# Performance work log

Measured on AMD Instinct MI355X. Metric: run time of the kernel, lower is better.

Reference implementation:

```python
import jax, jax.numpy as jnp
import numpy as np

N, IN_F, OUT_F = 8192, 512, 128
NEG = -1e11
LRELU_SLOPE = 0.01  # torch nn.LeakyReLU default


def setup_inputs() -> dict:
    key = jax.random.key(0)
    k1, k2, k3, k4, k5 = jax.random.split(key, 5)
    h = jax.random.normal(k1, (N, IN_F), dtype=jnp.float32)
    adj = jax.random.randint(k2, (N, N), 0, 2, dtype=jnp.int32)
    # nn.Linear weights, [out, in] convention; kaiming-uniform-ish init
    w = jax.random.uniform(k3, (OUT_F, IN_F), dtype=jnp.float32,
                           minval=-1.0, maxval=1.0) / np.sqrt(IN_F)
    a1 = jax.random.uniform(k4, (1, OUT_F), dtype=jnp.float32,
                            minval=-1.0, maxval=1.0) / np.sqrt(OUT_F)
    a2 = jax.random.uniform(k5, (1, OUT_F), dtype=jnp.float32,
                            minval=-1.0, maxval=1.0) / np.sqrt(OUT_F)
    return {"h": h, "adj": adj, "w": w, "a1": a1, "a2": a2}


def reference(h, adj, w, a1, a2):
    wh = h @ w.T                                # [N, out]
    wh1 = wh @ a1.T                             # [N, 1]
    wh2 = wh @ a2.T                             # [N, 1]
    e = wh1 + wh2.T                             # [N, N] broadcast add
    e = jnp.where(e > 0, e, LRELU_SLOPE * e)    # leaky relu
    scores = jnp.where(adj > 0, e, jnp.float32(NEG))
    attention = jax.nn.softmax(scores, axis=-1)  # [N, N]
    h_new = attention @ wh                       # [N, out]
    return jax.nn.elu(h_new)
```

## Files before the change

### kernel.cpp

```cpp
#include <hip/hip_runtime.h>
#include <hip/hip_bf16.h>
#include <cstdint>
#include <cstddef>

#define NV    8192
#define KIN   512
#define MOUT  128
#define LOG2E 1.4426950408889634f

typedef __attribute__((ext_vector_type(4))) float f32x4;
typedef __attribute__((ext_vector_type(8))) short short8;

__device__ __forceinline__ float elu1(float x) { return x > 0.f ? x : expm1f(x); }

__device__ __forceinline__ unsigned int pkbf2(float a, float b) {
  union { __hip_bfloat162 h2; unsigned int u; } r;
  r.h2 = __float22bfloat162_rn(make_float2(a, b));
  return r.u;
}

__global__ __launch_bounds__(256) void k_wh(const float* __restrict__ h,
                                            const float* __restrict__ w,
                                            const float* __restrict__ a1,
                                            const float* __restrict__ a2,
                                            unsigned short* __restrict__ fragB,
                                            float* __restrict__ wh1,
                                            float* __restrict__ wh2) {
  __shared__ __align__(16) float hT[64][36];
  __shared__ __align__(16) float wT[64][128];
  const int t = threadIdx.x;
  const int row0 = blockIdx.x * 32;
  const int hr = t >> 3, hu = t & 7;
  const int wc = t >> 1, whalf = t & 1;
  const int cg = t & 31, rg = t >> 5;
  const int c0 = cg * 4, r0 = rg * 4;
  float acc[4][4] = {};

  for (int kt = 0; kt < 8; ++kt) {
    const int k0 = kt * 64;
    __syncthreads();
#pragma unroll
    for (int v = 0; v < 8; ++v)
      hT[hu + 8 * v][hr] = h[(size_t)(row0 + hr) * KIN + k0 + hu + 8 * v];
#pragma unroll
    for (int mv = 0; mv < 8; ++mv) {
      const float4 wv4 = *(const float4*)&w[(size_t)wc * KIN + k0 + whalf * 32 + mv * 4];
      wT[whalf * 32 + mv * 4 + 0][wc] = wv4.x;
      wT[whalf * 32 + mv * 4 + 1][wc] = wv4.y;
      wT[whalf * 32 + mv * 4 + 2][wc] = wv4.z;
      wT[whalf * 32 + mv * 4 + 3][wc] = wv4.w;
    }
    __syncthreads();
#pragma unroll 8
    for (int kk = 0; kk < 64; ++kk) {
      const float4 hv = *(const float4*)&hT[kk][r0];
      const float4 wv4 = *(const float4*)&wT[kk][c0];
      const float hvv[4] = {hv.x, hv.y, hv.z, hv.w};
      const float wvv[4] = {wv4.x, wv4.y, wv4.z, wv4.w};
#pragma unroll
      for (int i = 0; i < 4; ++i)
#pragma unroll
        for (int j = 0; j < 4; ++j)
          acc[i][j] = fmaf(hvv[i], wvv[j], acc[i][j]);
    }
  }

  {
    const size_t jt = (size_t)(row0 >> 6);
    const int ks = (row0 >> 5) & 1;
    const int lg = rg >> 1, ebase = (rg & 1) * 4;
    const int cgf = cg >> 2;
    const size_t fbase = (((jt * 8 + cgf) * 2 + ks) * 64 + lg * 16) * 8 + ebase;
#pragma unroll
    for (int j = 0; j < 4; ++j) {
      const int l15 = (cg & 3) * 4 + j;
      uint2 o;
      o.x = pkbf2(acc[0][j], acc[1][j]);
      o.y = pkbf2(acc[2][j], acc[3][j]);
      *(uint2*)&fragB[fbase + (size_t)l15 * 8] = o;
    }
  }

  const float4 a1v = *(const float4*)&a1[c0];
  const float4 a2v = *(const float4*)&a2[c0];
#pragma unroll
  for (int i = 0; i < 4; ++i) {
    float s1 = acc[i][0] * a1v.x + acc[i][1] * a1v.y + acc[i][2] * a1v.z + acc[i][3] * a1v.w;
    float s2 = acc[i][0] * a2v.x + acc[i][1] * a2v.y + acc[i][2] * a2v.z + acc[i][3] * a2v.w;
#pragma unroll
    for (int off = 16; off > 0; off >>= 1) {
      s1 += __shfl_down(s1, off, 32);
      s2 += __shfl_down(s2, off, 32);
    }
    if (cg == 0) {
      wh1[row0 + r0 + i] = s1 * LOG2E;
      wh2[row0 + r0 + i] = s2 * LOG2E;
    }
  }
}

__global__ __launch_bounds__(256, 4) void k_attn_p(const unsigned short* __restrict__ fragB,
                                                   const int* __restrict__ adj,
                                                   const float* __restrict__ wh1l,
                                                   const float* __restrict__ wh2l,
                                                   float* __restrict__ out_p,
                                                   float* __restrict__ psum_p,
                                                   int ntiles) {
  extern __shared__ char smem[];
  const int t = threadIdx.x;
  const int i0 = blockIdx.x * 64;
  const int jbase = blockIdx.y * ntiles * 64;
  const int lane = t & 63, wv = t >> 6;
  const int ih = wv & 1, ch = wv >> 1;
  const int l15 = lane & 15, lg = lane >> 4;
  const int mstride = ntiles * 8 + 8;

  {
    const int nchunk = ntiles >> 4;
    for (int rr = 0; rr < 16; ++rr) {
      const int r = wv * 16 + rr;
      const int* ap = adj + (size_t)(i0 + r) * NV + jbase;
      for (int c = 0; c < nchunk; ++c) {
        const int chunk = c * 64 + lane;
        const int* bp = ap + chunk * 16;
        const int4 v0 = *(const int4*)(bp);
        const int4 v1 = *(const int4*)(bp + 4);
        const int4 v2 = *(const int4*)(bp + 8);
        const int4 v3 = *(const int4*)(bp + 12);
        const unsigned int m =
            (unsigned)(v0.x & 1)        | ((unsigned)(v0.y & 1) << 1)  |
            ((unsigned)(v0.z & 1) << 2) | ((unsigned)(v0.w & 1) << 3)  |
            ((unsigned)(v1.x & 1) << 4) | ((unsigned)(v1.y & 1) << 5)  |
            ((unsigned)(v1.z & 1) << 6) | ((unsigned)(v1.w & 1) << 7)  |
            ((unsigned)(v2.x & 1) << 8) | ((unsigned)(v2.y & 1) << 9)  |
            ((unsigned)(v2.z & 1) << 10)| ((unsigned)(v2.w & 1) << 11) |
            ((unsigned)(v3.x & 1) << 12)| ((unsigned)(v3.y & 1) << 13) |
            ((unsigned)(v3.z & 1) << 14)| ((unsigned)(v3.w & 1) << 15);
        *(unsigned short*)&smem[r * mstride + chunk * 2] = (unsigned short)m;
      }
    }
  }
  __syncthreads();

  const int rb = ih * 32;
  const float wh1a = wh1l[i0 + rb + l15];
  const float wh1b = wh1l[i0 + rb + 16 + l15];
  const char* mrowa = smem + (rb + l15) * mstride;
  const char* mrowb = smem + (rb + 16 + l15) * mstride;
  const unsigned short* bptr = fragB + (size_t)(jbase >> 6) * 8192 + ch * 4096 + lane * 8;
  const float* w2ptr = wh2l + jbase + lg * 8;

  f32x4 acc[2][4] = {};
  f32x4 accs[2] = {};
  short8 onesf;
#pragma unroll
  for (int e = 0; e < 8; ++e) onesf[e] = (short)0x3F80;

  uint2 m2a = *(const uint2*)&mrowa[0];
  uint2 m2b = *(const uint2*)&mrowb[0];
  short8 bf[8];
#pragma unroll
  for (int ks = 0; ks < 2; ++ks)
#pragma unroll
    for (int cgl = 0; cgl < 4; ++cgl)
      bf[ks * 4 + cgl] = *(const short8*)(bptr + cgl * 1024 + ks * 512);
  bptr += 8192;

  for (int it = 0; it < ntiles; ++it) {
    const unsigned int m16a = ((m2a.x >> (8 * lg)) & 0xFFu) |
                              (((m2a.y >> (8 * lg)) & 0xFFu) << 8);
    const unsigned int m16b = ((m2b.x >> (8 * lg)) & 0xFFu) |
                              (((m2b.y >> (8 * lg)) & 0xFFu) << 8);
    const float4 wq0 = *(const float4*)(w2ptr);
    const float4 wq1 = *(const float4*)(w2ptr + 4);
    const float4 wq2 = *(const float4*)(w2ptr + 32);
    const float4 wq3 = *(const float4*)(w2ptr + 36);
    w2ptr += 64;

    short8 afa[2], afb[2];
#pragma unroll
    for (int ks = 0; ks < 2; ++ks) {
      const float4 wa = ks ? wq2 : wq0;
      const float4 wb = ks ? wq3 : wq1;
      const float w2v[8] = {wa.x, wa.y, wa.z, wa.w, wb.x, wb.y, wb.z, wb.w};
      union { short8 s8; unsigned int u[4]; } pka, pkb;
#pragma unroll
      for (int e = 0; e < 4; ++e) {
        const float x0 = wh1a + w2v[2 * e];
        const float x1 = wh1a + w2v[2 * e + 1];
        const float y0 = wh1b + w2v[2 * e];
        const float y1 = wh1b + w2v[2 * e + 1];
        const float lx0 = fmaxf(x0, 0.01f * x0);
        const float lx1 = fmaxf(x1, 0.01f * x1);
        const float ly0 = fmaxf(y0, 0.01f * y0);
        const float ly1 = fmaxf(y1, 0.01f * y1);
        float px0 = __builtin_amdgcn_exp2f(lx0);
        float px1 = __builtin_amdgcn_exp2f(lx1);
        float py0 = __builtin_amdgcn_exp2f(ly0);
        float py1 = __builtin_amdgcn_exp2f(ly1);
        px0 = ((m16a >> (ks * 8 + 2 * e)) & 1u) ? px0 : 0.f;
        px1 = ((m16a >> (ks * 8 + 2 * e + 1)) & 1u) ? px1 : 0.f;
        py0 = ((m16b >> (ks * 8 + 2 * e)) & 1u) ? py0 : 0.f;
        py1 = ((m16b >> (ks * 8 + 2 * e + 1)) & 1u) ? py1 : 0.f;
        pka.u[e] = pkbf2(px0, px1);
        pkb.u[e] = pkbf2(py0, py1);
      }
      afa[ks] = pka.s8;
      afb[ks] = pkb.s8;
    }
    if (it + 1 < ntiles) {
      m2a = *(const uint2*)&mrowa[(it + 1) * 8];
      m2b = *(const uint2*)&mrowb[(it + 1) * 8];
    }
#pragma unroll
    for (int ks = 0; ks < 2; ++ks) {
      acc[0][0] = __builtin_amdgcn_mfma_f32_16x16x32_bf16(afa[ks], bf[ks * 4 + 0], acc[0][0], 0, 0, 0);
      acc[0][1] = __builtin_amdgcn_mfma_f32_16x16x32_bf16(afa[ks], bf[ks * 4 + 1], acc[0][1], 0, 0, 0);
      acc[0][2] = __builtin_amdgcn_mfma_f32_16x16x32_bf16(afa[ks], bf[ks * 4 + 2], acc[0][2], 0, 0, 0);
      acc[0][3] = __builtin_amdgcn_mfma_f32_16x16x32_bf16(afa[ks], bf[ks * 4 + 3], acc[0][3], 0, 0, 0);
      accs[0]   = __builtin_amdgcn_mfma_f32_16x16x32_bf16(afa[ks], onesf, accs[0], 0, 0, 0);
      acc[1][0] = __builtin_amdgcn_mfma_f32_16x16x32_bf16(afb[ks], bf[ks * 4 + 0], acc[1][0], 0, 0, 0);
      acc[1][1] = __builtin_amdgcn_mfma_f32_16x16x32_bf16(afb[ks], bf[ks * 4 + 1], acc[1][1], 0, 0, 0);
      acc[1][2] = __builtin_amdgcn_mfma_f32_16x16x32_bf16(afb[ks], bf[ks * 4 + 2], acc[1][2], 0, 0, 0);
      acc[1][3] = __builtin_amdgcn_mfma_f32_16x16x32_bf16(afb[ks], bf[ks * 4 + 3], acc[1][3], 0, 0, 0);
      accs[1]   = __builtin_amdgcn_mfma_f32_16x16x32_bf16(afb[ks], onesf, accs[1], 0, 0, 0);
    }
    if (it + 1 < ntiles) {
#pragma unroll
      for (int ks = 0; ks < 2; ++ks)
#pragma unroll
        for (int cgl = 0; cgl < 4; ++cgl)
          bf[ks * 4 + cgl] = *(const short8*)(bptr + cgl * 1024 + ks * 512);
      bptr += 8192;
    }
  }

  if (ch == 0 && l15 == 0) {
#pragma unroll
    for (int rg = 0; rg < 2; ++rg)
#pragma unroll
      for (int r = 0; r < 4; ++r)
        psum_p[(size_t)blockIdx.y * NV + i0 + rb + rg * 16 + lg * 4 + r] = accs[rg][r];
  }

#pragma unroll
  for (int rg = 0; rg < 2; ++rg) {
    const size_t ob = ((size_t)blockIdx.y * NV + i0 + rb + rg * 16) * MOUT + ch * 64;
#pragma unroll
    for (int cgl = 0; cgl < 4; ++cgl)
#pragma unroll
      for (int r = 0; r < 4; ++r)
        out_p[ob + (size_t)(lg * 4 + r) * MOUT + cgl * 16 + l15] = acc[rg][cgl][r];
  }
}

__global__ __launch_bounds__(256) void k_comb(const float* __restrict__ out_p,
                                              const float* __restrict__ psum_p,
                                              float* __restrict__ out, int S) {
  const int idx = (blockIdx.x * 256 + threadIdx.x) * 4;
  const int n = idx >> 7;
  float denom = 0.f;
  for (int s = 0; s < S; ++s) denom += psum_p[(size_t)s * NV + n];
  float4 acc = {0.f, 0.f, 0.f, 0.f};
  for (int s = 0; s < S; ++s) {
    const float4 v = *(const float4*)&out_p[(size_t)s * NV * MOUT + idx];
    acc.x += v.x; acc.y += v.y; acc.z += v.z; acc.w += v.w;
  }
  const float inv = 1.f / denom;
  float4 o;
  o.x = elu1(acc.x * inv);
  o.y = elu1(acc.y * inv);
  o.z = elu1(acc.z * inv);
  o.w = elu1(acc.w * inv);
  *(float4*)&out[idx] = o;
}

extern "C" void kernel_launch(void* const* d_in, const int* in_sizes, int n_in,
                              void* d_out, int out_size, void* d_ws, size_t ws_size,
                              hipStream_t stream) {
  const float* h  = (const float*)d_in[0];
  const int* adj  = (const int*)d_in[1];
  const float* w  = (const float*)d_in[2];
  const float* a1 = (const float*)d_in[3];
  const float* a2 = (const float*)d_in[4];
  float* out = (float*)d_out;

  char* ws = (char*)d_ws;
  unsigned short* fragB = (unsigned short*)ws;
  size_t off = (size_t)MOUT * NV * 2;
  float* wh1 = (float*)(ws + off); off += (size_t)NV * 4;
  float* wh2 = (float*)(ws + off); off += (size_t)NV * 4;
  float* psum_p = (float*)(ws + off); off += (size_t)8 * NV * 4;
  float* out_p = (float*)(ws + off);

  int S = 8;
  while (S > 1 && off + (size_t)S * NV * MOUT * 4 > ws_size) S >>= 1;
  const int ntiles = 128 / S;
  const size_t smbytes = (size_t)64 * (ntiles * 8 + 8);

  k_wh<<<NV / 32, 256, 0, stream>>>(h, w, a1, a2, fragB, wh1, wh2);
  k_attn_p<<<dim3(NV / 64, S), 256, smbytes, stream>>>(fragB, adj, wh1, wh2, out_p, psum_p, ntiles);
  k_comb<<<(NV * MOUT / 4) / 256, 256, 0, stream>>>(out_p, psum_p, out, S);
}
```

Baseline: 130.4 us.

## Pipeline adjacency mask loads with MFMA compute in attention kernel

Replaces the up-front adjacency-to-bitmask prologue, which loaded all mask bits before any compute began, with a software pipeline. Groups of adjacency rows are issued into registers two groups ahead and written to shared memory in stages, with a barrier every four tiles, so adjacency streaming overlaps the exp/MFMA work. It also hardcodes the split factor to 8 and uses a fixed static shared buffer, dropping the workspace-size fallback and the occupancy hint of 4 in launch bounds. The B-fragment prefetch across iterations is removed, so B loads now happen inside each tile.

```diff
diff --git a/kernel.cpp b/kernel.cpp
--- a/kernel.cpp
+++ b/kernel.cpp
@@ -99,56 +99,69 @@
   }
 }
 
-__global__ __launch_bounds__(256, 4) void k_attn_p(const unsigned short* __restrict__ fragB,
-                                                   const int* __restrict__ adj,
-                                                   const float* __restrict__ wh1l,
-                                                   const float* __restrict__ wh2l,
-                                                   float* __restrict__ out_p,
-                                                   float* __restrict__ psum_p,
-                                                   int ntiles) {
-  extern __shared__ char smem[];
+__device__ __forceinline__ void issue_grp(const int* __restrict__ base, int G, int wv,
+                                          int lane, int4 (&dst)[4]) {
+  const int c = G >> 2, rb4 = (G & 3) * 4;
+  const int r = wv * 16 + rb4 + (lane >> 4);
+  const int* p = base + (size_t)r * NV + c * 256 + (lane & 15) * 16;
+  dst[0] = *(const int4*)(p);
+  dst[1] = *(const int4*)(p + 4);
+  dst[2] = *(const int4*)(p + 8);
+  dst[3] = *(const int4*)(p + 12);
+}
+
+__device__ __forceinline__ void write_grp(char* sm, int G, int wv, int lane,
+                                          const int4 (&src)[4]) {
+  const int c = G >> 2, rb4 = (G & 3) * 4;
+  const int r = wv * 16 + rb4 + (lane >> 4);
+  unsigned int us = 0;
+#pragma unroll
+  for (int m = 0; m < 4; ++m) {
+    us |= (unsigned)(src[m].x & 1) << (4 * m);
+    us |= (unsigned)(src[m].y & 1) << (4 * m + 1);
+    us |= (unsigned)(src[m].z & 1) << (4 * m + 2);
+    us |= (unsigned)(src[m].w & 1) << (4 * m + 3);
+  }
+  const int l15q = lane & 15;
+  const int tile = c * 4 + (l15q >> 2), slot = l15q & 3;
+  *(unsigned short*)&sm[r * 136 + tile * 8 + slot * 2] = (unsigned short)us;
+}
+
+__global__ __launch_bounds__(256) void k_attn_p(const unsigned short* __restrict__ fragB,
+                                                const int* __restrict__ adj,
+                                                const float* __restrict__ wh1l,
+                                                const float* __restrict__ wh2l,
+                                                float* __restrict__ out_p,
+                                                float* __restrict__ psum_p) {
+  __shared__ char smask[64 * 136];
   const int t = threadIdx.x;
   const int i0 = blockIdx.x * 64;
-  const int jbase = blockIdx.y * ntiles * 64;
+  const int jbase = blockIdx.y * 1024;
   const int lane = t & 63, wv = t >> 6;
   const int ih = wv & 1, ch = wv >> 1;
   const int l15 = lane & 15, lg = lane >> 4;
-  const int mstride = ntiles * 8 + 8;
-
-  {
-    const int nchunk = ntiles >> 4;
-    for (int rr = 0; rr < 16; ++rr) {
-      const int r = wv * 16 + rr;
-      const int* ap = adj + (size_t)(i0 + r) * NV + jbase;
-      for (int c = 0; c < nchunk; ++c) {
-        const int chunk = c * 64 + lane;
-        const int* bp = ap + chunk * 16;
-        const int4 v0 = *(const int4*)(bp);
-        const int4 v1 = *(const int4*)(bp + 4);
-        const int4 v2 = *(const int4*)(bp + 8);
-        const int4 v3 = *(const int4*)(bp + 12);
-        const unsigned int m =
-            (unsigned)(v0.x & 1)        | ((unsigned)(v0.y & 1) << 1)  |
-            ((unsigned)(v0.z & 1) << 2) | ((unsigned)(v0.w & 1) << 3)  |
-            ((unsigned)(v1.x & 1) << 4) | ((unsigned)(v1.y & 1) << 5)  |
-            ((unsigned)(v1.z & 1) << 6) | ((unsigned)(v1.w & 1) << 7)  |
-            ((unsigned)(v2.x & 1) << 8) | ((unsigned)(v2.y & 1) << 9)  |
-            ((unsigned)(v2.z & 1) << 10)| ((unsigned)(v2.w & 1) << 11) |
-            ((unsigned)(v3.x & 1) << 12)| ((unsigned)(v3.y & 1) << 13) |
-            ((unsigned)(v3.z & 1) << 14)| ((unsigned)(v3.w & 1) << 15);
-        *(unsigned short*)&smem[r * mstride + chunk * 2] = (unsigned short)m;
-      }
-    }
-  }
-  __syncthreads();
+
+  const int* abase = adj + (size_t)i0 * NV + jbase;
+
+  int4 ga[4], gb[4];
+  issue_grp(abase, 0, wv, lane, ga);
+  issue_grp(abase, 1, wv, lane, gb);
+  write_grp(smask, 0, wv, lane, ga);
+  issue_grp(abase, 2, wv, lane, ga);
+  write_grp(smask, 1, wv, lane, gb);
+  issue_grp(abase, 3, wv, lane, gb);
+  write_grp(smask, 2, wv, lane, ga);
+  issue_grp(abase, 4, wv, lane, ga);
+  write_grp(smask, 3, wv, lane, gb);
+  issue_grp(abase, 5, wv, lane, gb);
 
   const int rb = ih * 32;
   const float wh1a = wh1l[i0 + rb + l15];
   const float wh1b = wh1l[i0 + rb + 16 + l15];
-  const char* mrowa = smem + (rb + l15) * mstride;
-  const char* mrowb = smem + (rb + 16 + l15) * mstride;
-  const unsigned short* bptr = fragB + (size_t)(jbase >> 6) * 8192 + ch * 4096 + lane * 8;
-  const float* w2ptr = wh2l + jbase + lg * 8;
+  const char* mrowa = smask + (rb + l15) * 136;
+  const char* mrowb = smask + (rb + 16 + l15) * 136;
+  const unsigned short* bbase = fragB + (size_t)(jbase >> 6) * 8192 + ch * 4096 + lane * 8;
+  const float* w2base = wh2l + jbase + lg * 8;
 
   f32x4 acc[2][4] = {};
   f32x4 accs[2] = {};
@@ -156,82 +169,85 @@
 #pragma unroll
   for (int e = 0; e < 8; ++e) onesf[e] = (short)0x3F80;
 
-  uint2 m2a = *(const uint2*)&mrowa[0];
-  uint2 m2b = *(const uint2*)&mrowb[0];
-  short8 bf[8];
-#pragma unroll
-  for (int ks = 0; ks < 2; ++ks)
-#pragma unroll
-    for (int cgl = 0; cgl < 4; ++cgl)
-      bf[ks * 4 + cgl] = *(const short8*)(bptr + cgl * 1024 + ks * 512);
-  bptr += 8192;
-
-  for (int it = 0; it < ntiles; ++it) {
-    const unsigned int m16a = ((m2a.x >> (8 * lg)) & 0xFFu) |
-                              (((m2a.y >> (8 * lg)) & 0xFFu) << 8);
-    const unsigned int m16b = ((m2b.x >> (8 * lg)) & 0xFFu) |
-                              (((m2b.y >> (8 * lg)) & 0xFFu) << 8);
-    const float4 wq0 = *(const float4*)(w2ptr);
-    const float4 wq1 = *(const float4*)(w2ptr + 4);
-    const float4 wq2 = *(const float4*)(w2ptr + 32);
-    const float4 wq3 = *(const float4*)(w2ptr + 36);
-    w2ptr += 64;
-
-    short8 afa[2], afb[2];
-#pragma unroll
-    for (int ks = 0; ks < 2; ++ks) {
-      const float4 wa = ks ? wq2 : wq0;
-      const float4 wb = ks ? wq3 : wq1;
-      const float w2v[8] = {wa.x, wa.y, wa.z, wa.w, wb.x, wb.y, wb.z, wb.w};
-      union { short8 s8; unsigned int u[4]; } pka, pkb;
-#pragma unroll
-      for (int e = 0; e < 4; ++e) {
-        const float x0 = wh1a + w2v[2 * e];
-        const float x1 = wh1a + w2v[2 * e + 1];
-        const float y0 = wh1b + w2v[2 * e];
-        const float y1 = wh1b + w2v[2 * e + 1];
-        const float lx0 = fmaxf(x0, 0.01f * x0);
-        const float lx1 = fmaxf(x1, 0.01f * x1);
-        const float ly0 = fmaxf(y0, 0.01f * y0);
-        const float ly1 = fmaxf(y1, 0.01f * y1);
-        float px0 = __builtin_amdgcn_exp2f(lx0);
-        float px1 = __builtin_amdgcn_exp2f(lx1);
-        float py0 = __builtin_amdgcn_exp2f(ly0);
-        float py1 = __builtin_amdgcn_exp2f(ly1);
-        px0 = ((m16a >> (ks * 8 + 2 * e)) & 1u) ? px0 : 0.f;
-        px1 = ((m16a >> (ks * 8 + 2 * e + 1)) & 1u) ? px1 : 0.f;
-        py0 = ((m16b >> (ks * 8 + 2 * e)) & 1u) ? py0 : 0.f;
-        py1 = ((m16b >> (ks * 8 + 2 * e + 1)) & 1u) ? py1 : 0.f;
-        pka.u[e] = pkbf2(px0, px1);
-        pkb.u[e] = pkbf2(py0, py1);
+  for (int q = 0; q < 4; ++q) {
+    __syncthreads();
+#pragma unroll
+    for (int tt = 0; tt < 4; ++tt) {
+      const int T = q * 4 + tt;
+      if (T + 4 < 16) {
+        if ((tt & 1) == 0) {
+          write_grp(smask, T + 4, wv, lane, ga);
+          if (T + 6 < 16) issue_grp(abase, T + 6, wv, lane, ga);
+        } else {
+          write_grp(smask, T + 4, wv, lane, gb);
+          if (T + 6 < 16) issue_grp(abase, T + 6, wv, lane, gb);
+        }
       }
-      afa[ks] = pka.s8;
-      afb[ks] = pkb.s8;
-    }
-    if (it + 1 < ntiles) {
-      m2a = *(const uint2*)&mrowa[(it + 1) * 8];
-      m2b = *(const uint2*)&mrowb[(it + 1) * 8];
-    }
-#pragma unroll
-    for (int ks = 0; ks < 2; ++ks) {
-      acc[0][0] = __builtin_amdgcn_mfma_f32_16x16x32_bf16(afa[ks], bf[ks * 4 + 0], acc[0][0], 0, 0, 0);
-      acc[0][1] = __builtin_amdgcn_mfma_f32_16x16x32_bf16(afa[ks], bf[ks * 4 + 1], acc[0][1], 0, 0, 0);
-      acc[0][2] = __builtin_amdgcn_mfma_f32_16x16x32_bf16(afa[ks], bf[ks * 4 + 2], acc[0][2], 0, 0, 0);
-      acc[0][3] = __builtin_amdgcn_mfma_f32_16x16x32_bf16(afa[ks], bf[ks * 4 + 3], acc[0][3], 0, 0, 0);
-      accs[0]   = __builtin_amdgcn_mfma_f32_16x16x32_bf16(afa[ks], onesf, accs[0], 0, 0, 0);
-      acc[1][0] = __builtin_amdgcn_mfma_f32_16x16x32_bf16(afb[ks], bf[ks * 4 + 0], acc[1][0], 0, 0, 0);
-      acc[1][1] = __builtin_amdgcn_mfma_f32_16x16x32_bf16(afb[ks], bf[ks * 4 + 1], acc[1][1], 0, 0, 0);
-      acc[1][2] = __builtin_amdgcn_mfma_f32_16x16x32_bf16(afb[ks], bf[ks * 4 + 2], acc[1][2], 0, 0, 0);
-      acc[1][3] = __builtin_amdgcn_mfma_f32_16x16x32_bf16(afb[ks], bf[ks * 4 + 3], acc[1][3], 0, 0, 0);
-      accs[1]   = __builtin_amdgcn_mfma_f32_16x16x32_bf16(afb[ks], onesf, accs[1], 0, 0, 0);
-    }
-    if (it + 1 < ntiles) {
-#pragma unroll
-      for (int ks = 0; ks < 2; ++ks)
-#pragma unroll
-        for (int cgl = 0; cgl < 4; ++cgl)
-          bf[ks * 4 + cgl] = *(const short8*)(bptr + cgl * 1024 + ks * 512);
-      bptr += 8192;
+      short8 bf[8];
+      {
+        const unsigned short* bp = bbase + (size_t)T * 8192;
+#pragma unroll
+        for (int ks = 0; ks < 2; ++ks)
+#pragma unroll
+          for (int cgl = 0; cgl < 4; ++cgl)
+            bf[ks * 4 + cgl] = *(const short8*)(bp + cgl * 1024 + ks * 512);
+      }
+      const uint2 m2a = *(const uint2*)&mrowa[T * 8];
+      const uint2 m2b = *(const uint2*)&mrowb[T * 8];
+      const float* w2p = w2base + T * 64;
+      const float4 wq0 = *(const float4*)(w2p);
+      const float4 wq1 = *(const float4*)(w2p + 4);
+      const float4 wq2 = *(const float4*)(w2p + 32);
+      const float4 wq3 = *(const float4*)(w2p + 36);
+      const unsigned int m16a = ((m2a.x >> (8 * lg)) & 0xFFu) |
+                                (((m2a.y >> (8 * lg)) & 0xFFu) << 8);
+      const unsigned int m16b = ((m2b.x >> (8 * lg)) & 0xFFu) |
+                                (((m2b.y >> (8 * lg)) & 0xFFu) << 8);
+
+      short8 afa[2], afb[2];
+#pragma unroll
+      for (int ks = 0; ks < 2; ++ks) {
+        const float4 wa = ks ? wq2 : wq0;
+        const float4 wb = ks ? wq3 : wq1;
+        const float w2v[8] = {wa.x, wa.y, wa.z, wa.w, wb.x, wb.y, wb.z, wb.w};
+        union { short8 s8; unsigned int u[4]; } pka, pkb;
+#pragma unroll
+        for (int e = 0; e < 4; ++e) {
+          const float x0 = wh1a + w2v[2 * e];
+          const float x1 = wh1a + w2v[2 * e + 1];
+          const float y0 = wh1b + w2v[2 * e];
+          const float y1 = wh1b + w2v[2 * e + 1];
+          const float lx0 = fmaxf(x0, 0.01f * x0);
+          const float lx1 = fmaxf(x1, 0.01f * x1);
+          const float ly0 = fmaxf(y0, 0.01f * y0);
+          const float ly1 = fmaxf(y1, 0.01f * y1);
+          float px0 = __builtin_amdgcn_exp2f(lx0);
+          float px1 = __builtin_amdgcn_exp2f(lx1);
+          float py0 = __builtin_amdgcn_exp2f(ly0);
+          float py1 = __builtin_amdgcn_exp2f(ly1);
+          px0 = ((m16a >> (ks * 8 + 2 * e)) & 1u) ? px0 : 0.f;
+          px1 = ((m16a >> (ks * 8 + 2 * e + 1)) & 1u) ? px1 : 0.f;
+          py0 = ((m16b >> (ks * 8 + 2 * e)) & 1u) ? py0 : 0.f;
+          py1 = ((m16b >> (ks * 8 + 2 * e + 1)) & 1u) ? py1 : 0.f;
+          pka.u[e] = pkbf2(px0, px1);
+          pkb.u[e] = pkbf2(py0, py1);
+        }
+        afa[ks] = pka.s8;
+        afb[ks] = pkb.s8;
+      }
+#pragma unroll
+      for (int ks = 0; ks < 2; ++ks) {
+        acc[0][0] = __builtin_amdgcn_mfma_f32_16x16x32_bf16(afa[ks], bf[ks * 4 + 0], acc[0][0], 0, 0, 0);
+        acc[0][1] = __builtin_amdgcn_mfma_f32_16x16x32_bf16(afa[ks], bf[ks * 4 + 1], acc[0][1], 0, 0, 0);
+        acc[0][2] = __builtin_amdgcn_mfma_f32_16x16x32_bf16(afa[ks], bf[ks * 4 + 2], acc[0][2], 0, 0, 0);
+        acc[0][3] = __builtin_amdgcn_mfma_f32_16x16x32_bf16(afa[ks], bf[ks * 4 + 3], acc[0][3], 0, 0, 0);
+        accs[0]   = __builtin_amdgcn_mfma_f32_16x16x32_bf16(afa[ks], onesf, accs[0], 0, 0, 0);
+        acc[1][0] = __builtin_amdgcn_mfma_f32_16x16x32_bf16(afb[ks], bf[ks * 4 + 0], acc[1][0], 0, 0, 0);
+        acc[1][1] = __builtin_amdgcn_mfma_f32_16x16x32_bf16(afb[ks], bf[ks * 4 + 1], acc[1][1], 0, 0, 0);
+        acc[1][2] = __builtin_amdgcn_mfma_f32_16x16x32_bf16(afb[ks], bf[ks * 4 + 2], acc[1][2], 0, 0, 0);
+        acc[1][3] = __builtin_amdgcn_mfma_f32_16x16x32_bf16(afb[ks], bf[ks * 4 + 3], acc[1][3], 0, 0, 0);
+        accs[1]   = __builtin_amdgcn_mfma_f32_16x16x32_bf16(afb[ks], onesf, accs[1], 0, 0, 0);
+      }
     }
   }
 
@@ -293,12 +309,7 @@
   float* psum_p = (float*)(ws + off); off += (size_t)8 * NV * 4;
   float* out_p = (float*)(ws + off);
 
-  int S = 8;
-  while (S > 1 && off + (size_t)S * NV * MOUT * 4 > ws_size) S >>= 1;
-  const int ntiles = 128 / S;
-  const size_t smbytes = (size_t)64 * (ntiles * 8 + 8);
-
   k_wh<<<NV / 32, 256, 0, stream>>>(h, w, a1, a2, fragB, wh1, wh2);
-  k_attn_p<<<dim3(NV / 64, S), 256, smbytes, stream>>>(fragB, adj, wh1, wh2, out_p, psum_p, ntiles);
-  k_comb<<<(NV * MOUT / 4) / 256, 256, 0, stream>>>(out_p, psum_p, out, S);
-}
+  k_attn_p<<<dim3(NV / 64, 8), 256, 0, stream>>>(fragB, adj, wh1, wh2, out_p, psum_p);
+  k_comb<<<(NV * MOUT / 4) / 256, 256, 0, stream>>>(out_p, psum_p, out, 8);
+}
```

Result: no change. 131.0 us (+0.5%).
